# Kernel tuning notes

Hardware: AMD Instinct MI355X
Metric: run time of the kernel (lower is better)

Reference implementation:

```python
import jax, jax.numpy as jnp
import numpy as np

B, T, F1, F2 = 16384, 5, 300, 251
IN, H = 551, 128

def setup_inputs() -> dict:
    key = jax.random.key(0)
    ks = jax.random.split(key, 16)
    s = 0.05
    return {
        "x1": jax.random.normal(ks[0], (B, T, F1), jnp.float32),
        "x2": jax.random.normal(ks[1], (B, T, F2), jnp.float32),
        "W_ih": jax.random.normal(ks[2], (4 * H, IN), jnp.float32) * s,
        "W_hh": jax.random.normal(ks[3], (4 * H, H), jnp.float32) * s,
        "b_ih": jax.random.normal(ks[4], (4 * H,), jnp.float32) * s,
        "b_hh": jax.random.normal(ks[5], (4 * H,), jnp.float32) * s,
        "W1": jax.random.normal(ks[6], (531, H * T), jnp.float32) * s,
        "b1": jax.random.normal(ks[7], (531,), jnp.float32) * s,
        "W2": jax.random.normal(ks[8], (256, 531), jnp.float32) * s,
        "b2": jax.random.normal(ks[9], (256,), jnp.float32) * s,
        "W3": jax.random.normal(ks[10], (64, 256), jnp.float32) * s,
        "b3": jax.random.normal(ks[11], (64,), jnp.float32) * s,
        "W4": jax.random.normal(ks[12], (2, 64), jnp.float32) * s,
        "b4": jax.random.normal(ks[13], (2,), jnp.float32) * s,
    }

def _lstm(x, W_ih, W_hh, b_ih, b_hh):
    # x: [B, T, IN] -> outputs [B, T, H]; PyTorch gate order i, f, g, o
    xg = jnp.einsum('bti,gi->btg', x, W_ih) + b_ih + b_hh  # [B, T, 4H]
    xg = jnp.transpose(xg, (1, 0, 2))  # [T, B, 4H]
    h0 = jnp.zeros((x.shape[0], H), x.dtype)
    c0 = jnp.zeros((x.shape[0], H), x.dtype)

    def step(carry, xg_t):
        h, c = carry
        g = xg_t + h @ W_hh.T  # [B, 4H]
        i, f, gg, o = jnp.split(g, 4, axis=-1)
        c = jax.nn.sigmoid(f) * c + jax.nn.sigmoid(i) * jnp.tanh(gg)
        h = jax.nn.sigmoid(o) * jnp.tanh(c)
        return (h, c), h

    _, hs = jax.lax.scan(step, (h0, c0), xg)  # hs: [T, B, H]
    return jnp.transpose(hs, (1, 0, 2))

def reference(x1, x2, W_ih, W_hh, b_ih, b_hh, W1, b1, W2, b2, W3, b3, W4, b4):
    x = jnp.concatenate((x1, x2), axis=2)  # [B, T, 551]
    h = _lstm(x, W_ih, W_hh, b_ih, b_hh)   # [B, T, H]
    h = h.reshape(h.shape[0], T * H)
    h = jax.nn.relu(h @ W1.T + b1)
    h = jax.nn.relu(h @ W2.T + b2)
    h = jax.nn.relu(h @ W3.T + b3)
    logits = h @ W4.T + b4
    return jax.nn.softmax(logits, axis=1)
```

## Files before the change

kernel.cpp:

```cpp
#include <hip/hip_runtime.h>
#include <hip/hip_bf16.h>


typedef short  short8  __attribute__((ext_vector_type(8)));
typedef short  short4v __attribute__((ext_vector_type(4)));
typedef float  f32x4   __attribute__((ext_vector_type(4)));

#define MFMA(a, b, c) __builtin_amdgcn_mfma_f32_16x16x32_bf16((a), (b), (c), 0, 0, 0)

__device__ __forceinline__ short f2bs(float f) {
    __hip_bfloat16 h = __float2bfloat16(f);
    union { __hip_bfloat16 h; short s; } u; u.h = h; return u.s;
}
__device__ __forceinline__ float b2f(short s) {
    union { unsigned u; float f; } v; v.u = ((unsigned)(unsigned short)s) << 16; return v.f;
}
__device__ __forceinline__ float sigf(float x)  { return 1.f / (1.f + __expf(-x)); }
__device__ __forceinline__ float mytanh(float x){ return 2.f / (1.f + __expf(-2.f * x)) - 1.f; }

#define BB     16384
#define TT     5
#define F1     300
#define F2     251
#define INF    551
#define KP     576
#define G4     512
#define HH     128
#define FLAT   640
#define L1N    531
#define L1P    576
#define L1KP   544
#define L2N    256
#define L3N    64

#define O_WIH  0u
#define O_WHH  589824u
#define O_W1   720896u
#define O_W2   1458176u
#define O_W3   1736704u
#define O_BG   1769472u
#define O_B1   1771520u
#define O_XG   1773824u
#define O_HS   85659904u
#define WS_NEED 106631424u

__device__ __forceinline__ void pack_b(const float* __restrict__ W, short* __restrict__ dst,
                                       int i, int tpn, int Nsrc, int Ksrc, int ldw)
{
    int tile = i >> 9, rem = i & 511, lane = rem >> 3, jj = rem & 7;
    int tn = tile / tpn, tk = tile - tn * tpn;
    int n = tn * 16 + (lane & 15);
    int k = tk * 32 + (lane >> 4) * 8 + jj;
    float v = (n < Nsrc && k < Ksrc) ? W[n * ldw + k] : 0.f;
    dst[i] = f2bs(v);
}

__global__ void prep_kernel(
    const float* __restrict__ W_ih, const float* __restrict__ W_hh,
    const float* __restrict__ b_ih, const float* __restrict__ b_hh,
    const float* __restrict__ W1,   const float* __restrict__ b1,
    const float* __restrict__ W2,   const float* __restrict__ W3,
    short* __restrict__ Wihp, short* __restrict__ Whhp, float* __restrict__ biasg,
    short* __restrict__ W1p,  float* __restrict__ b1p,  short* __restrict__ W2p,
    short* __restrict__ W3p)
{
    const int N0 = G4 * KP;
    const int N1 = N0 + G4 * HH;
    const int N2 = N1 + L1P * FLAT;
    const int N3 = N2 + L2N * L1KP;
    const int N4 = N3 + L3N * L2N;
    const int N5 = N4 + G4;
    const int N6 = N5 + L1P;
    const int stride = gridDim.x * blockDim.x;
    for (int i = blockIdx.x * blockDim.x + threadIdx.x; i < N6; i += stride) {
        if (i < N0)      pack_b(W_ih, Wihp, i,       18, G4,  INF, INF);
        else if (i < N1) pack_b(W_hh, Whhp, i - N0,   4, G4,  HH,  HH);
        else if (i < N2) pack_b(W1,   W1p,  i - N1,  20, L1N, FLAT, FLAT);
        else if (i < N3) pack_b(W2,   W2p,  i - N2,  17, L2N, L1N, L1N);
        else if (i < N4) pack_b(W3,   W3p,  i - N3,   8, L3N, L2N, L2N);
        else if (i < N5) { int j = i - N4; biasg[j] = b_ih[j] + b_hh[j]; }
        else             { int j = i - N5; b1p[j] = (j < L1N) ? b1[j] : 0.f; }
    }
}

__device__ __forceinline__ float4 load_chunk4(const float* __restrict__ x1,
                                              const float* __restrict__ x2,
                                              int brow, int t, int c)
{
    if (c < F1) {
        return *(const float4*)(x1 + (brow * TT + t) * F1 + c);
    }
    float4 r;
    int base = (brow * TT + t) * F2 + (c - F1);
    r.x = (c + 0 < INF) ? x2[base + 0] : 0.f;
    r.y = (c + 1 < INF) ? x2[base + 1] : 0.f;
    r.z = (c + 2 < INF) ? x2[base + 2] : 0.f;
    r.w = (c + 3 < INF) ? x2[base + 3] : 0.f;
    return r;
}

__global__ __launch_bounds__(512, 4) void k1_xgemm(
    const float* __restrict__ x1, const float* __restrict__ x2,
    const short* __restrict__ Wihp, const float* __restrict__ biasg,
    short* __restrict__ xg)
{
    __shared__ __align__(16) short At[64][296];
    const int tid  = threadIdx.x;
    const int w    = tid >> 6;
    const int lane = tid & 63;
    const int quad = lane >> 4;
    const int c16  = lane & 15;
    const int m0   = blockIdx.x * 64;
    const int t    = m0 >> 14;
    const int bb   = m0 & 16383;

    f32x4 acc[4][4];
#pragma unroll
    for (int mt = 0; mt < 4; ++mt)
#pragma unroll
        for (int nt = 0; nt < 4; ++nt)
            acc[mt][nt] = (f32x4){0.f, 0.f, 0.f, 0.f};

    const int srow  = tid >> 3;
    const int kslot = tid & 7;

    for (int half = 0; half < 2; ++half) {
        __syncthreads();
        {
            int brow = bb + srow;
#pragma unroll
            for (int c = 0; c < 9; ++c) {
                int kl = c * 32 + kslot * 4;
                float4 v = load_chunk4(x1, x2, brow, t, half * 288 + kl);
                short4v s;
                s[0] = f2bs(v.x); s[1] = f2bs(v.y); s[2] = f2bs(v.z); s[3] = f2bs(v.w);
                *(short4v*)&At[srow][kl] = s;
            }
        }
        __syncthreads();
#pragma unroll
        for (int ks = 0; ks < 9; ++ks) {
            short8 a[4];
#pragma unroll
            for (int mt = 0; mt < 4; ++mt)
                a[mt] = *(const short8*)&At[mt * 16 + c16][ks * 32 + quad * 8];
#pragma unroll
            for (int nt = 0; nt < 4; ++nt) {
                int tk = half * 9 + ks;
                short8 b = *(const short8*)&Wihp[(((w * 4 + nt) * 18 + tk) << 9) + lane * 8];
#pragma unroll
                for (int mt = 0; mt < 4; ++mt)
                    acc[mt][nt] = MFMA(a[mt], b, acc[mt][nt]);
            }
        }
    }
#pragma unroll
    for (int nt = 0; nt < 4; ++nt) {
        float bv = biasg[w * 64 + nt * 16 + c16];
#pragma unroll
        for (int mt = 0; mt < 4; ++mt) {
            short4v o;
#pragma unroll
            for (int r = 0; r < 4; ++r) o[r] = f2bs(acc[mt][nt][r] + bv);
            int tm = (m0 >> 4) + mt, tn = w * 4 + nt;
            *(short4v*)&xg[((tm * 32 + tn) << 8) + lane * 4] = o;
        }
    }
}

__global__ __launch_bounds__(512, 2) void k2_rec(
    const short* __restrict__ Whhp, const short* __restrict__ xg,
    short* __restrict__ hs)
{
    __shared__ __align__(16) short hb[2][32][136];
    const int tid  = threadIdx.x;
    const int w    = tid >> 6;
    const int lane = tid & 63;
    const int quad = lane >> 4;
    const int c16  = lane & 15;
    const int btile = blockIdx.x * 2;

    short8 bfr[4][4];
#pragma unroll
    for (int g = 0; g < 4; ++g)
#pragma unroll
        for (int ks = 0; ks < 4; ++ks)
            bfr[g][ks] = *(const short8*)&Whhp[((((g * 8 + w) * 4) + ks) << 9) + lane * 8];

    float cst[2][4];
#pragma unroll
    for (int mt = 0; mt < 2; ++mt)
#pragma unroll
        for (int r = 0; r < 4; ++r) cst[mt][r] = 0.f;

    const int j = w * 16 + c16;

    for (int t = 0; t < TT; ++t) {
        short4v xq[2][4];
#pragma unroll
        for (int mt = 0; mt < 2; ++mt)
#pragma unroll
            for (int g = 0; g < 4; ++g)
                xq[mt][g] = *(const short4v*)
                    &xg[((((t << 10) + btile + mt) * 32 + (g * 8 + w)) << 8) + lane * 4];

        f32x4 acc[2][4];
#pragma unroll
        for (int mt = 0; mt < 2; ++mt)
#pragma unroll
            for (int g = 0; g < 4; ++g)
                acc[mt][g] = (f32x4){0.f, 0.f, 0.f, 0.f};

        if (t > 0) {
            const short (*cur)[136] = hb[(t - 1) & 1];
#pragma unroll
            for (int ks = 0; ks < 4; ++ks) {
                short8 a[2];
#pragma unroll
                for (int mt = 0; mt < 2; ++mt)
                    a[mt] = *(const short8*)&cur[mt * 16 + c16][ks * 32 + quad * 8];
#pragma unroll
                for (int mt = 0; mt < 2; ++mt)
#pragma unroll
                    for (int g = 0; g < 4; ++g)
                        acc[mt][g] = MFMA(a[mt], bfr[g][ks], acc[mt][g]);
            }
        }

        short (*nxt)[136] = hb[t & 1];
#pragma unroll
        for (int mt = 0; mt < 2; ++mt) {
#pragma unroll
            for (int r = 0; r < 4; ++r) {
                int m = mt * 16 + quad * 4 + r;
                float gi = acc[mt][0][r] + b2f(xq[mt][0][r]);
                float gf = acc[mt][1][r] + b2f(xq[mt][1][r]);
                float gg = acc[mt][2][r] + b2f(xq[mt][2][r]);
                float go = acc[mt][3][r] + b2f(xq[mt][3][r]);
                float cn = sigf(gf) * cst[mt][r] + sigf(gi) * mytanh(gg);
                cst[mt][r] = cn;
                nxt[m][j] = f2bs(sigf(go) * mytanh(cn));
            }
        }
        __syncthreads();
        {
            int tm = w >> 2, kt = w & 3;
            short8 v = *(const short8*)&nxt[tm * 16 + c16][kt * 32 + quad * 8];
            *(short8*)&hs[(((btile + tm) * 20 + t * 4 + kt) << 9) + lane * 8] = v;
        }
    }
}

__global__ __launch_bounds__(256, 2) void mlp_kernel(
    const short* __restrict__ hs,
    const short* __restrict__ W1p, const float* __restrict__ b1p,
    const short* __restrict__ W2p, const float* __restrict__ b2,
    const short* __restrict__ W3p, const float* __restrict__ b3,
    const float* __restrict__ W4,  const float* __restrict__ b4,
    float* __restrict__ out)
{
    __shared__ __align__(16) short a1[32][584];
    __shared__ __align__(16) short a2[32][264];
    __shared__ __align__(16) short a3[32][72];
    const int tid  = threadIdx.x;
    const int w    = tid >> 6;
    const int lane = tid & 63;
    const int quad = lane >> 4;
    const int c16  = lane & 15;
    const int m0   = blockIdx.x * 32;
    const int mtile = blockIdx.x * 2;

    {
        f32x4 acc[2][9];
#pragma unroll
        for (int mt = 0; mt < 2; ++mt)
#pragma unroll
            for (int i = 0; i < 9; ++i)
                acc[mt][i] = (f32x4){0.f, 0.f, 0.f, 0.f};
#pragma unroll 4
        for (int ks = 0; ks < 20; ++ks) {
            short8 a[2];
#pragma unroll
            for (int mt = 0; mt < 2; ++mt)
                a[mt] = *(const short8*)&hs[(((mtile + mt) * 20 + ks) << 9) + lane * 8];
#pragma unroll
            for (int i = 0; i < 9; ++i) {
                short8 b = *(const short8*)&W1p[(((w * 9 + i) * 20 + ks) << 9) + lane * 8];
                acc[0][i] = MFMA(a[0], b, acc[0][i]);
                acc[1][i] = MFMA(a[1], b, acc[1][i]);
            }
        }
#pragma unroll
        for (int i = 0; i < 9; ++i) {
            int n = (w * 9 + i) * 16 + c16;
            float bv = b1p[n];
#pragma unroll
            for (int mt = 0; mt < 2; ++mt)
#pragma unroll
                for (int r = 0; r < 4; ++r) {
                    int m = mt * 16 + quad * 4 + r;
                    float v = acc[mt][i][r] + bv;
                    a1[m][n] = f2bs(v > 0.f ? v : 0.f);
                }
        }
    }
    __syncthreads();

    {
        f32x4 acc[2][4];
#pragma unroll
        for (int mt = 0; mt < 2; ++mt)
#pragma unroll
            for (int i = 0; i < 4; ++i)
                acc[mt][i] = (f32x4){0.f, 0.f, 0.f, 0.f};
#pragma unroll 4
        for (int ks = 0; ks < 17; ++ks) {
            short8 a[2];
#pragma unroll
            for (int mt = 0; mt < 2; ++mt)
                a[mt] = *(const short8*)&a1[mt * 16 + c16][ks * 32 + quad * 8];
#pragma unroll
            for (int i = 0; i < 4; ++i) {
                short8 b = *(const short8*)&W2p[(((w * 4 + i) * 17 + ks) << 9) + lane * 8];
                acc[0][i] = MFMA(a[0], b, acc[0][i]);
                acc[1][i] = MFMA(a[1], b, acc[1][i]);
            }
        }
#pragma unroll
        for (int i = 0; i < 4; ++i) {
            int n = (w * 4 + i) * 16 + c16;
            float bv = b2[n];
#pragma unroll
            for (int mt = 0; mt < 2; ++mt)
#pragma unroll
                for (int r = 0; r < 4; ++r) {
                    int m = mt * 16 + quad * 4 + r;
                    float v = acc[mt][i][r] + bv;
                    a2[m][n] = f2bs(v > 0.f ? v : 0.f);
                }
        }
    }
    __syncthreads();

    {
        f32x4 acc[2];
        acc[0] = (f32x4){0.f, 0.f, 0.f, 0.f};
        acc[1] = (f32x4){0.f, 0.f, 0.f, 0.f};
#pragma unroll
        for (int ks = 0; ks < 8; ++ks) {
            short8 a[2];
#pragma unroll
            for (int mt = 0; mt < 2; ++mt)
                a[mt] = *(const short8*)&a2[mt * 16 + c16][ks * 32 + quad * 8];
            short8 b = *(const short8*)&W3p[((w * 8 + ks) << 9) + lane * 8];
            acc[0] = MFMA(a[0], b, acc[0]);
            acc[1] = MFMA(a[1], b, acc[1]);
        }
        int n = w * 16 + c16;
        float bv = b3[n];
#pragma unroll
        for (int mt = 0; mt < 2; ++mt)
#pragma unroll
            for (int r = 0; r < 4; ++r) {
                int m = mt * 16 + quad * 4 + r;
                float v = acc[mt][r] + bv;
                a3[m][n] = f2bs(v > 0.f ? v : 0.f);
            }
    }
    __syncthreads();

    if (tid < 64) {
        int m   = tid >> 1;
        int cls = tid & 1;
        float s = b4[cls];
#pragma unroll 8
        for (int k = 0; k < 64; ++k)
            s += b2f(a3[m][k]) * W4[cls * 64 + k];
        float other = __shfl_xor(s, 1);
        float p = 1.f / (1.f + __expf(other - s));
        out[(m0 + m) * 2 + cls] = p;
    }
}

extern "C" void kernel_launch(void* const* d_in, const int* in_sizes, int n_in,
                              void* d_out, int out_size, void* d_ws, size_t ws_size,
                              hipStream_t stream)
{
    (void)in_sizes; (void)n_in; (void)out_size;
    if (ws_size < (size_t)WS_NEED) return;

    const float* x1   = (const float*)d_in[0];
    const float* x2   = (const float*)d_in[1];
    const float* W_ih = (const float*)d_in[2];
    const float* W_hh = (const float*)d_in[3];
    const float* b_ih = (const float*)d_in[4];
    const float* b_hh = (const float*)d_in[5];
    const float* W1   = (const float*)d_in[6];
    const float* b1   = (const float*)d_in[7];
    const float* W2   = (const float*)d_in[8];
    const float* b2   = (const float*)d_in[9];
    const float* W3   = (const float*)d_in[10];
    const float* b3   = (const float*)d_in[11];
    const float* W4   = (const float*)d_in[12];
    const float* b4   = (const float*)d_in[13];

    char* ws = (char*)d_ws;
    short* Wihp  = (short*)(ws + O_WIH);
    short* Whhp  = (short*)(ws + O_WHH);
    short* W1p   = (short*)(ws + O_W1);
    short* W2p   = (short*)(ws + O_W2);
    short* W3p   = (short*)(ws + O_W3);
    float* biasg = (float*)(ws + O_BG);
    float* b1p   = (float*)(ws + O_B1);
    short* xg    = (short*)(ws + O_XG);
    short* hsb   = (short*)(ws + O_HS);

    prep_kernel<<<3461, 256, 0, stream>>>(W_ih, W_hh, b_ih, b_hh, W1, b1, W2, W3,
                                          Wihp, Whhp, biasg, W1p, b1p, W2p, W3p);
    k1_xgemm<<<1280, 512, 0, stream>>>(x1, x2, Wihp, biasg, xg);
    k2_rec<<<512, 512, 0, stream>>>(Whhp, xg, hsb);
    mlp_kernel<<<512, 256, 0, stream>>>(hsb, W1p, b1p, W2p, b2, W3p, b3, W4, b4,
                                        (float*)d_out);
}
```

Baseline: 366.6 us.

## Double-buffer LDS in input GEMM and prefetch next K-chunk during MFMA

```diff
diff --git a/kernel.cpp b/kernel.cpp
--- a/kernel.cpp
+++ b/kernel.cpp
@@ -83,19 +83,16 @@
     }
 }
 
-__device__ __forceinline__ float4 load_chunk4(const float* __restrict__ x1,
-                                              const float* __restrict__ x2,
-                                              int brow, int t, int c)
-{
-    if (c < F1) {
-        return *(const float4*)(x1 + (brow * TT + t) * F1 + c);
-    }
+__device__ __forceinline__ float4 ld4(const float* __restrict__ x1r,
+                                      const float* __restrict__ x2r, int c)
+{
+    if (c + 3 < F1) return *(const float4*)(x1r + c);
+    if (c + 3 < INF) return *(const float4*)(x2r + (c - F1));
     float4 r;
-    int base = (brow * TT + t) * F2 + (c - F1);
-    r.x = (c + 0 < INF) ? x2[base + 0] : 0.f;
-    r.y = (c + 1 < INF) ? x2[base + 1] : 0.f;
-    r.z = (c + 2 < INF) ? x2[base + 2] : 0.f;
-    r.w = (c + 3 < INF) ? x2[base + 3] : 0.f;
+    r.x = (c + 0 < INF) ? x2r[c - F1 + 0] : 0.f;
+    r.y = (c + 1 < INF) ? x2r[c - F1 + 1] : 0.f;
+    r.z = (c + 2 < INF) ? x2r[c - F1 + 2] : 0.f;
+    r.w = (c + 3 < INF) ? x2r[c - F1 + 3] : 0.f;
     return r;
 }
 
@@ -104,7 +101,7 @@
     const short* __restrict__ Wihp, const float* __restrict__ biasg,
     short* __restrict__ xg)
 {
-    __shared__ __align__(16) short At[64][296];
+    __shared__ __align__(16) short At[2][64][72];
     const int tid  = threadIdx.x;
     const int w    = tid >> 6;
     const int lane = tid & 63;
@@ -114,6 +111,11 @@
     const int t    = m0 >> 14;
     const int bb   = m0 & 16383;
 
+    const int srow  = tid >> 3;
+    const int kslot = tid & 7;
+    const float* x1r = x1 + ((size_t)(bb + srow) * TT + t) * F1;
+    const float* x2r = x2 + ((size_t)(bb + srow) * TT + t) * F2;
+
     f32x4 acc[4][4];
 #pragma unroll
     for (int mt = 0; mt < 4; ++mt)
@@ -121,39 +123,49 @@
         for (int nt = 0; nt < 4; ++nt)
             acc[mt][nt] = (f32x4){0.f, 0.f, 0.f, 0.f};
 
-    const int srow  = tid >> 3;
-    const int kslot = tid & 7;
-
-    for (int half = 0; half < 2; ++half) {
-        __syncthreads();
-        {
-            int brow = bb + srow;
-#pragma unroll
-            for (int c = 0; c < 9; ++c) {
-                int kl = c * 32 + kslot * 4;
-                float4 v = load_chunk4(x1, x2, brow, t, half * 288 + kl);
-                short4v s;
-                s[0] = f2bs(v.x); s[1] = f2bs(v.y); s[2] = f2bs(v.z); s[3] = f2bs(v.w);
-                *(short4v*)&At[srow][kl] = s;
-            }
-        }
-        __syncthreads();
-#pragma unroll
-        for (int ks = 0; ks < 9; ++ks) {
+    {
+        int c = kslot * 8;
+        float4 v0 = *(const float4*)(x1r + c);
+        float4 v1 = *(const float4*)(x1r + c + 4);
+        short8 s;
+        s[0] = f2bs(v0.x); s[1] = f2bs(v0.y); s[2] = f2bs(v0.z); s[3] = f2bs(v0.w);
+        s[4] = f2bs(v1.x); s[5] = f2bs(v1.y); s[6] = f2bs(v1.z); s[7] = f2bs(v1.w);
+        *(short8*)&At[0][srow][kslot * 8] = s;
+    }
+    __syncthreads();
+
+    for (int ch = 0; ch < 9; ++ch) {
+        const int cur = ch & 1;
+        float4 q0, q1;
+        if (ch < 8) {
+            int c = (ch + 1) * 64 + kslot * 8;
+            q0 = ld4(x1r, x2r, c);
+            q1 = ld4(x1r, x2r, c + 4);
+        }
+#pragma unroll
+        for (int ks = 0; ks < 2; ++ks) {
             short8 a[4];
 #pragma unroll
             for (int mt = 0; mt < 4; ++mt)
-                a[mt] = *(const short8*)&At[mt * 16 + c16][ks * 32 + quad * 8];
+                a[mt] = *(const short8*)&At[cur][mt * 16 + c16][ks * 32 + quad * 8];
+            const int tk = ch * 2 + ks;
 #pragma unroll
             for (int nt = 0; nt < 4; ++nt) {
-                int tk = half * 9 + ks;
                 short8 b = *(const short8*)&Wihp[(((w * 4 + nt) * 18 + tk) << 9) + lane * 8];
 #pragma unroll
                 for (int mt = 0; mt < 4; ++mt)
                     acc[mt][nt] = MFMA(a[mt], b, acc[mt][nt]);
             }
         }
-    }
+        if (ch < 8) {
+            short8 s;
+            s[0] = f2bs(q0.x); s[1] = f2bs(q0.y); s[2] = f2bs(q0.z); s[3] = f2bs(q0.w);
+            s[4] = f2bs(q1.x); s[5] = f2bs(q1.y); s[6] = f2bs(q1.z); s[7] = f2bs(q1.w);
+            *(short8*)&At[cur ^ 1][srow][kslot * 8] = s;
+        }
+        __syncthreads();
+    }
+
 #pragma unroll
     for (int nt = 0; nt < 4; ++nt) {
         float bv = biasg[w * 64 + nt * 16 + c16];
```

Result: slower. 377.0 us (+2.9%).

## Pipeline input-projection GEMM with async LDS weight loads and larger M tile

Applied to the files above, without the earlier changes.

```diff
diff --git a/kernel.cpp b/kernel.cpp
--- a/kernel.cpp
+++ b/kernel.cpp
@@ -7,6 +7,9 @@
 typedef float  f32x4   __attribute__((ext_vector_type(4)));
 
 #define MFMA(a, b, c) __builtin_amdgcn_mfma_f32_16x16x32_bf16((a), (b), (c), 0, 0, 0)
+#define WAITV(N) asm volatile("s_waitcnt vmcnt(" #N ")" ::: "memory")
+#define MEMF()   asm volatile("" ::: "memory")
+#define BAR()    __builtin_amdgcn_s_barrier()
 
 __device__ __forceinline__ short f2bs(float f) {
     __hip_bfloat16 h = __float2bfloat16(f);
@@ -17,6 +20,12 @@
 }
 __device__ __forceinline__ float sigf(float x)  { return 1.f / (1.f + __expf(-x)); }
 __device__ __forceinline__ float mytanh(float x){ return 2.f / (1.f + __expf(-2.f * x)) - 1.f; }
+
+__device__ __forceinline__ void gload16(const short* g, short* l) {
+    __builtin_amdgcn_global_load_lds(
+        (const __attribute__((address_space(1))) void*)g,
+        (__attribute__((address_space(3))) void*)l, 16, 0, 0);
+}
 
 #define BB     16384
 #define TT     5
@@ -83,82 +92,121 @@
     }
 }
 
-__device__ __forceinline__ float4 load_chunk4(const float* __restrict__ x1,
-                                              const float* __restrict__ x2,
-                                              int brow, int t, int c)
-{
-    if (c < F1) {
-        return *(const float4*)(x1 + (brow * TT + t) * F1 + c);
-    }
-    float4 r;
-    int base = (brow * TT + t) * F2 + (c - F1);
-    r.x = (c + 0 < INF) ? x2[base + 0] : 0.f;
-    r.y = (c + 1 < INF) ? x2[base + 1] : 0.f;
-    r.z = (c + 2 < INF) ? x2[base + 2] : 0.f;
-    r.w = (c + 3 < INF) ? x2[base + 3] : 0.f;
-    return r;
-}
-
-__global__ __launch_bounds__(512, 4) void k1_xgemm(
+__device__ __forceinline__ float4 ld4u(const float* __restrict__ x1r,
+                                       const float* __restrict__ x2r, int c)
+{
+    int c2 = c - F1;
+    c2 = (c2 < F2) ? c2 : 0;
+    const float* p = (c < F1) ? (x1r + c) : (x2r + c2);
+    return *(const float4*)p;
+}
+
+__device__ __forceinline__ void k1_step(const short* __restrict__ Ab8,
+                                        const short* __restrict__ Bb8,
+                                        int w, int lane, f32x4 (&acc)[8][4])
+{
+    short8 a[8];
+#pragma unroll
+    for (int mt = 0; mt < 8; ++mt)
+        a[mt] = *(const short8*)&Ab8[mt * 512 + lane * 8];
+#pragma unroll
+    for (int nt = 0; nt < 4; ++nt) {
+        short8 b = *(const short8*)&Bb8[(w * 4 + nt) * 512 + lane * 8];
+#pragma unroll
+        for (int mt = 0; mt < 8; ++mt)
+            acc[mt][nt] = MFMA(a[mt], b, acc[mt][nt]);
+    }
+}
+
+__global__ __launch_bounds__(512, 2) void k1_xgemm(
     const float* __restrict__ x1, const float* __restrict__ x2,
     const short* __restrict__ Wihp, const float* __restrict__ biasg,
     short* __restrict__ xg)
 {
-    __shared__ __align__(16) short At[64][296];
+    __shared__ __align__(16) short Ab[2][8][512];
+    __shared__ __align__(16) short Bb[3][32][512];
     const int tid  = threadIdx.x;
     const int w    = tid >> 6;
     const int lane = tid & 63;
-    const int quad = lane >> 4;
     const int c16  = lane & 15;
-    const int m0   = blockIdx.x * 64;
+    const int kq   = lane >> 4;
+    const int m0   = blockIdx.x * 128;
     const int t    = m0 >> 14;
     const int bb   = m0 & 16383;
 
-    f32x4 acc[4][4];
-#pragma unroll
-    for (int mt = 0; mt < 4; ++mt)
+    const int arow = bb + w * 16 + c16;
+    const float* x1r = x1 + ((size_t)arow * TT + t) * F1;
+    const float* x2r = x2 + ((size_t)arow * TT + t) * F2;
+    const int ac0 = kq * 8;
+
+    f32x4 acc[8][4];
+#pragma unroll
+    for (int mt = 0; mt < 8; ++mt)
 #pragma unroll
         for (int nt = 0; nt < 4; ++nt)
             acc[mt][nt] = (f32x4){0.f, 0.f, 0.f, 0.f};
 
-    const int srow  = tid >> 3;
-    const int kslot = tid & 7;
-
-    for (int half = 0; half < 2; ++half) {
-        __syncthreads();
+#pragma unroll
+    for (int i = 0; i < 4; ++i) {
+        int tn = w * 4 + i;
+        gload16(Wihp + ((tn * 18 + 0) << 9) + lane * 8, &Bb[0][tn][lane * 8]);
+    }
+    float4 p0 = ld4u(x1r, x2r, ac0), p1 = ld4u(x1r, x2r, ac0 + 4);
+#pragma unroll
+    for (int i = 0; i < 4; ++i) {
+        int tn = w * 4 + i;
+        gload16(Wihp + ((tn * 18 + 1) << 9) + lane * 8, &Bb[1][tn][lane * 8]);
+    }
+    float4 r0 = ld4u(x1r, x2r, 32 + ac0), r1 = ld4u(x1r, x2r, 32 + ac0 + 4);
+    {
+        short8 v;
+        v[0]=f2bs(p0.x); v[1]=f2bs(p0.y); v[2]=f2bs(p0.z); v[3]=f2bs(p0.w);
+        v[4]=f2bs(p1.x); v[5]=f2bs(p1.y); v[6]=f2bs(p1.z); v[7]=f2bs(p1.w);
+        *(short8*)&Ab[0][w][lane * 8] = v;
+    }
+    WAITV(6); BAR(); MEMF();
+
+    int bS = 2, bR = 0;
+    for (int s = 0; s < 16; ++s) {
+        const int tk = s + 2;
+#pragma unroll
+        for (int i = 0; i < 4; ++i) {
+            int tn = w * 4 + i;
+            gload16(Wihp + ((tn * 18 + tk) << 9) + lane * 8, &Bb[bS][tn][lane * 8]);
+        }
+        int c = tk * 32 + ac0;
+        float4 n0 = ld4u(x1r, x2r, c), n1 = ld4u(x1r, x2r, c + 4);
+
+        k1_step(&Ab[s & 1][0][0], &Bb[bR][0][0], w, lane, acc);
+
         {
-            int brow = bb + srow;
-#pragma unroll
-            for (int c = 0; c < 9; ++c) {
-                int kl = c * 32 + kslot * 4;
-                float4 v = load_chunk4(x1, x2, brow, t, half * 288 + kl);
-                short4v s;
-                s[0] = f2bs(v.x); s[1] = f2bs(v.y); s[2] = f2bs(v.z); s[3] = f2bs(v.w);
-                *(short4v*)&At[srow][kl] = s;
-            }
-        }
-        __syncthreads();
-#pragma unroll
-        for (int ks = 0; ks < 9; ++ks) {
-            short8 a[4];
-#pragma unroll
-            for (int mt = 0; mt < 4; ++mt)
-                a[mt] = *(const short8*)&At[mt * 16 + c16][ks * 32 + quad * 8];
-#pragma unroll
-            for (int nt = 0; nt < 4; ++nt) {
-                int tk = half * 9 + ks;
-                short8 b = *(const short8*)&Wihp[(((w * 4 + nt) * 18 + tk) << 9) + lane * 8];
-#pragma unroll
-                for (int mt = 0; mt < 4; ++mt)
-                    acc[mt][nt] = MFMA(a[mt], b, acc[mt][nt]);
-            }
-        }
-    }
+            short8 v;
+            v[0]=f2bs(r0.x); v[1]=f2bs(r0.y); v[2]=f2bs(r0.z); v[3]=f2bs(r0.w);
+            v[4]=f2bs(r1.x); v[5]=f2bs(r1.y); v[6]=f2bs(r1.z); v[7]=f2bs(r1.w);
+            *(short8*)&Ab[(s + 1) & 1][w][lane * 8] = v;
+        }
+        r0 = n0; r1 = n1;
+        WAITV(6); BAR(); MEMF();
+        bS = (bS == 2) ? 0 : bS + 1;
+        bR = (bR == 2) ? 0 : bR + 1;
+    }
+
+    k1_step(&Ab[0][0][0], &Bb[1][0][0], w, lane, acc);
+    {
+        short8 v;
+        v[0]=f2bs(r0.x); v[1]=f2bs(r0.y); v[2]=f2bs(r0.z); v[3]=f2bs(r0.w);
+        v[4]=f2bs(r1.x); v[5]=f2bs(r1.y); v[6]=f2bs(r1.z); v[7]=f2bs(r1.w);
+        *(short8*)&Ab[1][w][lane * 8] = v;
+    }
+    WAITV(0); BAR(); MEMF();
+
+    k1_step(&Ab[1][0][0], &Bb[2][0][0], w, lane, acc);
+
 #pragma unroll
     for (int nt = 0; nt < 4; ++nt) {
         float bv = biasg[w * 64 + nt * 16 + c16];
 #pragma unroll
-        for (int mt = 0; mt < 4; ++mt) {
+        for (int mt = 0; mt < 8; ++mt) {
             short4v o;
 #pragma unroll
             for (int r = 0; r < 4; ++r) o[r] = f2bs(acc[mt][nt][r] + bv);
@@ -417,7 +465,7 @@
 
     prep_kernel<<<3461, 256, 0, stream>>>(W_ih, W_hh, b_ih, b_hh, W1, b1, W2, W3,
                                           Wihp, Whhp, biasg, W1p, b1p, W2p, W3p);
-    k1_xgemm<<<1280, 512, 0, stream>>>(x1, x2, Wihp, biasg, xg);
+    k1_xgemm<<<640, 512, 0, stream>>>(x1, x2, Wihp, biasg, xg);
     k2_rec<<<512, 512, 0, stream>>>(Whhp, xg, hsb);
     mlp_kernel<<<512, 256, 0, stream>>>(hsb, W1p, b1p, W2p, b2, W3p, b3, W4, b4,
                                         (float*)d_out);
```

Result: slower. 380.9 us (+3.9%).

## Restructure input-projection GEMM into 128x128 K-step tiles with LDS-staged weights

Applied to the files above, without the earlier changes.

```diff
diff --git a/kernel.cpp b/kernel.cpp
--- a/kernel.cpp
+++ b/kernel.cpp
@@ -7,6 +7,10 @@
 typedef float  f32x4   __attribute__((ext_vector_type(4)));
 
 #define MFMA(a, b, c) __builtin_amdgcn_mfma_f32_16x16x32_bf16((a), (b), (c), 0, 0, 0)
+#define WAITV(N) asm volatile("s_waitcnt vmcnt(" #N ")" ::: "memory")
+#define LGKM0()  asm volatile("s_waitcnt lgkmcnt(0)" ::: "memory")
+#define MEMF()   asm volatile("" ::: "memory")
+#define BAR()    __builtin_amdgcn_s_barrier()
 
 __device__ __forceinline__ short f2bs(float f) {
     __hip_bfloat16 h = __float2bfloat16(f);
@@ -17,6 +21,12 @@
 }
 __device__ __forceinline__ float sigf(float x)  { return 1.f / (1.f + __expf(-x)); }
 __device__ __forceinline__ float mytanh(float x){ return 2.f / (1.f + __expf(-2.f * x)) - 1.f; }
+
+__device__ __forceinline__ void gload16(const void* g, void* l) {
+    __builtin_amdgcn_global_load_lds(
+        (const __attribute__((address_space(1))) void*)g,
+        (__attribute__((address_space(3))) void*)l, 16, 0, 0);
+}
 
 #define BB     16384
 #define TT     5
@@ -55,6 +65,18 @@
     dst[i] = f2bs(v);
 }
 
+__device__ __forceinline__ void pack_bih(const float* __restrict__ W, short* __restrict__ dst,
+                                         int i)
+{
+    int tile = i >> 9, rem = i & 511, lane = rem >> 3, jj = rem & 7;
+    int tn = tile / 18, tk = tile - tn * 18;
+    int n = tn * 16 + (lane & 15);
+    int k = tk * 32 + (lane >> 4) * 8 + jj;
+    int keff = (k <= 546) ? k : (k >= 548 && k <= 551) ? (k - 1) : -1;
+    float v = (keff >= 0) ? W[n * INF + keff] : 0.f;
+    dst[i] = f2bs(v);
+}
+
 __global__ void prep_kernel(
     const float* __restrict__ W_ih, const float* __restrict__ W_hh,
     const float* __restrict__ b_ih, const float* __restrict__ b_hh,
@@ -73,7 +95,7 @@
     const int N6 = N5 + L1P;
     const int stride = gridDim.x * blockDim.x;
     for (int i = blockIdx.x * blockDim.x + threadIdx.x; i < N6; i += stride) {
-        if (i < N0)      pack_b(W_ih, Wihp, i,       18, G4,  INF, INF);
+        if (i < N0)      pack_bih(W_ih, Wihp, i);
         else if (i < N1) pack_b(W_hh, Whhp, i - N0,   4, G4,  HH,  HH);
         else if (i < N2) pack_b(W1,   W1p,  i - N1,  20, L1N, FLAT, FLAT);
         else if (i < N3) pack_b(W2,   W2p,  i - N2,  17, L2N, L1N, L1N);
@@ -83,36 +105,41 @@
     }
 }
 
-__device__ __forceinline__ float4 load_chunk4(const float* __restrict__ x1,
-                                              const float* __restrict__ x2,
-                                              int brow, int t, int c)
-{
-    if (c < F1) {
-        return *(const float4*)(x1 + (brow * TT + t) * F1 + c);
-    }
-    float4 r;
-    int base = (brow * TT + t) * F2 + (c - F1);
-    r.x = (c + 0 < INF) ? x2[base + 0] : 0.f;
-    r.y = (c + 1 < INF) ? x2[base + 1] : 0.f;
-    r.z = (c + 2 < INF) ? x2[base + 2] : 0.f;
-    r.w = (c + 3 < INF) ? x2[base + 3] : 0.f;
-    return r;
-}
-
-__global__ __launch_bounds__(512, 4) void k1_xgemm(
+__device__ __forceinline__ float4 ld4r(const float* __restrict__ x1r,
+                                       const float* __restrict__ x2r, int c)
+{
+    const float* p = (c < F1) ? (x1r + c) : (x2r + (c - F1));
+    return *(const float4*)p;
+}
+
+__global__ __launch_bounds__(256, 3) void k1_xgemm(
     const float* __restrict__ x1, const float* __restrict__ x2,
     const short* __restrict__ Wihp, const float* __restrict__ biasg,
     short* __restrict__ xg)
 {
-    __shared__ __align__(16) short At[64][296];
+    __shared__ __align__(16) short As[128][32];
+    __shared__ __align__(16) short Bs[8][512];
     const int tid  = threadIdx.x;
     const int w    = tid >> 6;
     const int lane = tid & 63;
-    const int quad = lane >> 4;
     const int c16  = lane & 15;
-    const int m0   = blockIdx.x * 64;
-    const int t    = m0 >> 14;
-    const int bb   = m0 & 16383;
+    const int kq   = lane >> 4;
+    const int wm   = w >> 1, wn = w & 1;
+
+    const int id  = blockIdx.x;
+    const int mp  = (id & 7) * 80 + ((id >> 3) >> 2);
+    const int nb  = (id >> 3) & 3;
+    const int m0  = mp * 128;
+    const int t   = m0 >> 14;
+    const int bb  = m0 & 16383;
+
+    const int sr = tid >> 1, sh = tid & 1;
+    const int arow = bb + sr;
+    const float* x1r = x1 + ((size_t)arow * TT + t) * F1;
+    const float* x2r = x2 + ((size_t)arow * TT + t) * F2;
+    const int fA = (sr >> 1) & 3;
+    short* d0 = &As[sr][(((sh << 1)    ) ^ fA) << 3];
+    short* d1 = &As[sr][(((sh << 1) | 1) ^ fA) << 3];
 
     f32x4 acc[4][4];
 #pragma unroll
@@ -121,48 +148,68 @@
         for (int nt = 0; nt < 4; ++nt)
             acc[mt][nt] = (f32x4){0.f, 0.f, 0.f, 0.f};
 
-    const int srow  = tid >> 3;
-    const int kslot = tid & 7;
-
-    for (int half = 0; half < 2; ++half) {
-        __syncthreads();
+    for (int s = 0; s < 18; ++s) {
+        BAR(); MEMF();
+#pragma unroll
+        for (int i2 = 0; i2 < 2; ++i2) {
+            int tnl = w * 2 + i2;
+            gload16(Wihp + (((nb * 8 + tnl) * 18 + s) << 9) + lane * 8,
+                    &Bs[tnl][0]);
+        }
+        float4 q0, q1, q2, q3;
+        if (s < 17) {
+            int c0 = s * 32 + sh * 16;
+            q0 = ld4r(x1r, x2r, c0);
+            q1 = ld4r(x1r, x2r, c0 + 4);
+            q2 = ld4r(x1r, x2r, c0 + 8);
+            q3 = ld4r(x1r, x2r, c0 + 12);
+        } else {
+            if (sh == 0) {
+                q0 = *(const float4*)(x2r + 244);
+                q1 = *(const float4*)(x2r + 247);
+            } else {
+                q0 = (float4){0.f, 0.f, 0.f, 0.f};
+                q1 = q0;
+            }
+            q2 = (float4){0.f, 0.f, 0.f, 0.f};
+            q3 = q2;
+        }
         {
-            int brow = bb + srow;
-#pragma unroll
-            for (int c = 0; c < 9; ++c) {
-                int kl = c * 32 + kslot * 4;
-                float4 v = load_chunk4(x1, x2, brow, t, half * 288 + kl);
-                short4v s;
-                s[0] = f2bs(v.x); s[1] = f2bs(v.y); s[2] = f2bs(v.z); s[3] = f2bs(v.w);
-                *(short4v*)&At[srow][kl] = s;
-            }
-        }
-        __syncthreads();
-#pragma unroll
-        for (int ks = 0; ks < 9; ++ks) {
-            short8 a[4];
+            short8 v0, v1;
+            v0[0] = f2bs(q0.x); v0[1] = f2bs(q0.y); v0[2] = f2bs(q0.z); v0[3] = f2bs(q0.w);
+            v0[4] = f2bs(q1.x); v0[5] = f2bs(q1.y); v0[6] = f2bs(q1.z); v0[7] = f2bs(q1.w);
+            v1[0] = f2bs(q2.x); v1[1] = f2bs(q2.y); v1[2] = f2bs(q2.z); v1[3] = f2bs(q2.w);
+            v1[4] = f2bs(q3.x); v1[5] = f2bs(q3.y); v1[6] = f2bs(q3.z); v1[7] = f2bs(q3.w);
+            *(short8*)d0 = v0;
+            *(short8*)d1 = v1;
+        }
+        WAITV(0); LGKM0(); BAR(); MEMF();
+
+        short8 a[4];
+#pragma unroll
+        for (int mt = 0; mt < 4; ++mt) {
+            int r = (wm * 4 + mt) * 16 + c16;
+            a[mt] = *(const short8*)&As[r][(kq ^ ((r >> 1) & 3)) << 3];
+        }
+#pragma unroll
+        for (int nt = 0; nt < 4; ++nt) {
+            short8 b = *(const short8*)&Bs[wn * 4 + nt][lane * 8];
 #pragma unroll
             for (int mt = 0; mt < 4; ++mt)
-                a[mt] = *(const short8*)&At[mt * 16 + c16][ks * 32 + quad * 8];
-#pragma unroll
-            for (int nt = 0; nt < 4; ++nt) {
-                int tk = half * 9 + ks;
-                short8 b = *(const short8*)&Wihp[(((w * 4 + nt) * 18 + tk) << 9) + lane * 8];
-#pragma unroll
-                for (int mt = 0; mt < 4; ++mt)
-                    acc[mt][nt] = MFMA(a[mt], b, acc[mt][nt]);
-            }
-        }
-    }
+                acc[mt][nt] = MFMA(a[mt], b, acc[mt][nt]);
+        }
+    }
+
 #pragma unroll
     for (int nt = 0; nt < 4; ++nt) {
-        float bv = biasg[w * 64 + nt * 16 + c16];
+        int tn = nb * 8 + wn * 4 + nt;
+        float bv = biasg[tn * 16 + c16];
 #pragma unroll
         for (int mt = 0; mt < 4; ++mt) {
             short4v o;
 #pragma unroll
             for (int r = 0; r < 4; ++r) o[r] = f2bs(acc[mt][nt][r] + bv);
-            int tm = (m0 >> 4) + mt, tn = w * 4 + nt;
+            int tm = (m0 >> 4) + wm * 4 + mt;
             *(short4v*)&xg[((tm * 32 + tn) << 8) + lane * 4] = o;
         }
     }
@@ -417,7 +464,7 @@
 
     prep_kernel<<<3461, 256, 0, stream>>>(W_ih, W_hh, b_ih, b_hh, W1, b1, W2, W3,
                                           Wihp, Whhp, biasg, W1p, b1p, W2p, W3p);
-    k1_xgemm<<<1280, 512, 0, stream>>>(x1, x2, Wihp, biasg, xg);
+    k1_xgemm<<<2560, 256, 0, stream>>>(x1, x2, Wihp, biasg, xg);
     k2_rec<<<512, 512, 0, stream>>>(Whhp, xg, hsb);
     mlp_kernel<<<512, 256, 0, stream>>>(hsb, W1p, b1p, W2p, b2, W3p, b3, W4, b4,
                                         (float*)d_out);
```

Result: slower. 398.9 us (+8.8%).
